# Kernel tuning notes

Hardware: AMD Instinct MI355X
Metric: run time of the kernel (lower is better)

The kernel has to match this reference:

```python
import jax, jax.numpy as jnp
import numpy as np
import math

B, T, N_EMBD, HEAD_SIZE = 8, 2048, 768, 128


def setup_inputs() -> dict:
    key = jax.random.key(0)
    ks = jax.random.split(key, 7)
    s = 0.02
    return {
        "x": jax.random.normal(ks[0], (B, T, N_EMBD), dtype=jnp.float32),
        "Wq": jax.random.normal(ks[1], (N_EMBD, HEAD_SIZE), dtype=jnp.float32) * s,
        "bq": jax.random.normal(ks[2], (HEAD_SIZE,), dtype=jnp.float32) * s,
        "Wk": jax.random.normal(ks[3], (N_EMBD, HEAD_SIZE), dtype=jnp.float32) * s,
        "bk": jax.random.normal(ks[4], (HEAD_SIZE,), dtype=jnp.float32) * s,
        "Wv": jax.random.normal(ks[5], (N_EMBD, HEAD_SIZE), dtype=jnp.float32) * s,
        "bv": jax.random.normal(ks[6], (HEAD_SIZE,), dtype=jnp.float32) * s,
    }


def reference(x, Wq, bq, Wk, bk, Wv, bv):
    # x: [B, T, n_embd]
    Tlen = x.shape[1]
    q = x @ Wq + bq  # [B, T, hs]
    k = x @ Wk + bk
    v = x @ Wv + bv
    scores = jnp.einsum('bqd,bkd->bqk', q, k)  # [B, T, T]
    causal = jnp.tril(jnp.ones((Tlen, Tlen), dtype=bool))
    # original masks with -inf first, then divides by sqrt(head_size); -inf/scale == -inf,
    # so mask-then-scale is mathematically identical.
    scores = jnp.where(causal, scores, -jnp.inf) / math.sqrt(q.shape[-1])
    weights = jax.nn.softmax(scores, axis=-1)
    # dropout p=0.0 (inference/reference) -> identity
    out = jnp.einsum('bqk,bkd->bqd', weights, v)  # [B, T, hs]
    return out
```

## Files before the change

kernel.cpp:

```cpp
#include <hip/hip_runtime.h>

#define B_ 8
#define T_ 2048
#define E_ 768
#define D_ 128
#define SCALE2 (0.08838834764831845f * 1.4426950408889634f)

typedef _Float16 h8 __attribute__((ext_vector_type(8)));
typedef _Float16 h4 __attribute__((ext_vector_type(4)));
typedef _Float16 h2 __attribute__((ext_vector_type(2)));
typedef float f4 __attribute__((ext_vector_type(4)));

typedef __attribute__((address_space(1))) unsigned int as1_u32;
typedef __attribute__((address_space(3))) unsigned int as3_u32;

__device__ __forceinline__ void gl_lds16(const void* g, void* l) {
    __builtin_amdgcn_global_load_lds((const as1_u32*)g, (as3_u32*)l, 16, 0, 0);
}

__global__ __launch_bounds__(256) void w_prep(
    const float* __restrict__ Wq, const float* __restrict__ Wk,
    const float* __restrict__ Wv, _Float16* __restrict__ Wh)
{
    __shared__ float tile[64][129];
    const int y = blockIdx.x / 12, kc = blockIdx.x % 12;
    const float* W = (y == 0) ? Wq : (y == 1) ? Wk : Wv;
    const int k0 = kc * 64, t = threadIdx.x;
#pragma unroll
    for (int i = 0; i < 32; ++i) {
        const int idx = i * 256 + t;
        tile[idx >> 7][idx & 127] = W[(size_t)(k0 + (idx >> 7)) * D_ + (idx & 127)];
    }
    __syncthreads();
    const int n = t >> 1, hf = t & 1;
#pragma unroll
    for (int j = 0; j < 4; ++j) {
        const int kk = hf * 32 + j * 8;
        h8 hv;
#pragma unroll
        for (int e = 0; e < 8; ++e) hv[e] = (_Float16)tile[kk + e][n];
        *(h8*)&Wh[(size_t)(y * 128 + n) * E_ + k0 + kk] = hv;
    }
}

__global__ __launch_bounds__(512, 1) void qkv_fused(
    const float* __restrict__ x, const _Float16* __restrict__ Wh,
    const float* __restrict__ bq, const float* __restrict__ bk,
    const float* __restrict__ bv,
    _Float16* __restrict__ Qh, _Float16* __restrict__ Kh,
    _Float16* __restrict__ Vt)
{
    __shared__ _Float16 As[2][64 * 64];
    __shared__ _Float16 Bs[2][384 * 64];

    const int t = threadIdx.x;
    const int lane = t & 63, w = t >> 6;
    const int quad = lane >> 4, col = lane & 15;
    const int m0 = blockIdx.x * 64;

    f4 acc[4][3];
#pragma unroll
    for (int mt = 0; mt < 4; ++mt)
#pragma unroll
        for (int nt = 0; nt < 3; ++nt) acc[mt][nt] = (f4){0.f, 0.f, 0.f, 0.f};

    const int brl = lane >> 3, bc = lane & 7;
    const int xr_ = t >> 3, xcb = (t & 7) * 8;

    float4 xv[2];

#define LOAD_X(kb)                                                          \
    {   const float* xr = &x[(size_t)(m0 + xr_) * E_ + (kb) + xcb];         \
        xv[0] = *(const float4*)(xr);                                       \
        xv[1] = *(const float4*)(xr + 4);                                   }

#define STAGE_B(dst, kb)                                                    \
    _Pragma("unroll")                                                       \
    for (int i = 0; i < 6; ++i) {                                           \
        const int R = w * 48 + i * 8;                                       \
        const int r = R + brl;                                              \
        gl_lds16(Wh + (size_t)r * E_ + (kb) + 8 * (bc ^ (r & 7)), &(dst)[R * 64]); }

#define WRITE_A(dst)                                                        \
    _Pragma("unroll")                                                       \
    for (int i = 0; i < 2; ++i) {                                           \
        h4 hv; hv[0] = (_Float16)xv[i].x; hv[1] = (_Float16)xv[i].y;        \
        hv[2] = (_Float16)xv[i].z; hv[3] = (_Float16)xv[i].w;               \
        const int kk4 = xcb + 4 * i;                                        \
        *(h4*)&(dst)[xr_ * 64 + (((kk4 >> 3) ^ (xr_ & 7)) << 3) + (kk4 & 7)] = hv; }

    LOAD_X(0);
    STAGE_B(Bs[0], 0);
    asm volatile("s_waitcnt vmcnt(6)" ::: "memory");
    WRITE_A(As[0]);
    asm volatile("s_waitcnt vmcnt(0) lgkmcnt(0)" ::: "memory");
    __builtin_amdgcn_s_barrier();

#pragma unroll 2
    for (int it = 0; it < 12; ++it) {
        const int c = it & 1;
        if (it < 11) {
            LOAD_X((it + 1) * 64);
            STAGE_B(Bs[c ^ 1], (it + 1) * 64);
        }
#pragma unroll
        for (int ks = 0; ks < 2; ++ks) {
            const int sc = ((ks << 2) + quad) ^ (col & 7);
            h8 a[4], bf[3];
#pragma unroll
            for (int mt = 0; mt < 4; ++mt)
                a[mt] = *(const h8*)&As[c][(mt * 16 + col) * 64 + (sc << 3)];
#pragma unroll
            for (int nt = 0; nt < 3; ++nt)
                bf[nt] = *(const h8*)&Bs[c][(w * 48 + nt * 16 + col) * 64 + (sc << 3)];
#pragma unroll
            for (int mt = 0; mt < 4; ++mt)
#pragma unroll
                for (int nt = 0; nt < 3; ++nt)
                    acc[mt][nt] = __builtin_amdgcn_mfma_f32_16x16x32_f16(
                        a[mt], bf[nt], acc[mt][nt], 0, 0, 0);
        }
        if (it < 11) {
            asm volatile("s_waitcnt vmcnt(6)" ::: "memory");
            WRITE_A(As[c ^ 1]);
            asm volatile("s_waitcnt vmcnt(0) lgkmcnt(0)" ::: "memory");
            __builtin_amdgcn_s_barrier();
        }
    }

    const float* bp[3] = {bq, bk, bv};
    _Float16* Cs = &Bs[0][0];
#pragma unroll
    for (int nt = 0; nt < 3; ++nt) {
        const int n16 = w * 48 + nt * 16;
        const int y = n16 >> 7, nl = n16 & 127;
        const float bb = bp[y][nl + col];
#pragma unroll
        for (int mt = 0; mt < 4; ++mt)
#pragma unroll
            for (int reg = 0; reg < 4; ++reg) {
                const int m = mt * 16 + quad * 4 + reg;
                Cs[m * 384 + n16 + col] = (_Float16)(acc[mt][nt][reg] + bb);
            }
    }
    __syncthreads();

    {
        const int m = t >> 3, seg = t & 7;
#pragma unroll
        for (int j = 0; j < 4; ++j) {
            const int n = seg * 8 + j * 64;
            const h8 v = *(const h8*)&Cs[m * 384 + n];
            if (n < 128) *(h8*)&Qh[(size_t)(m0 + m) * D_ + n] = v;
            else         *(h8*)&Kh[(size_t)(m0 + m) * D_ + (n - 128)] = v;
        }
    }
    {
        const int vn = t & 127, part = t >> 7;
        const int bidx = m0 >> 11, tt0 = m0 & 2047;
#pragma unroll
        for (int j = 0; j < 2; ++j) {
            const int ms = part * 16 + j * 8;
            h8 hv;
#pragma unroll
            for (int e = 0; e < 8; ++e) hv[e] = Cs[(ms + e) * 384 + 256 + vn];
            *(h8*)&Vt[((size_t)bidx * D_ + vn) * T_ + tt0 + ms] = hv;
        }
    }
#undef LOAD_X
#undef STAGE_B
#undef WRITE_A
}

__global__ __launch_bounds__(256, 2) void flash_attn(
    const _Float16* __restrict__ Qh,
    const _Float16* __restrict__ Kh,
    const _Float16* __restrict__ Vt,
    float* __restrict__ out)
{
    __shared__ __align__(16) char smem[70656];
    _Float16* Ks = (_Float16*)smem;
    _Float16* Vs = (_Float16*)(smem + 32768);
    _Float16* Pb = (_Float16*)(smem + 65536);

    const int t = threadIdx.x, lane = t & 63, w = t >> 6;
    const int quad = lane >> 4, col = lane & 15;
    const int id = blockIdx.x;
    const int b = id & 7;
    const int k6 = id >> 3;
    const int j32 = (k6 < 32) ? (63 - k6) : (k6 - 32);
    const int qw = w & 1, kh = w >> 1;
    const int qbase = j32 * 32;
    const int qrow0 = qbase + qw * 16;
    const int nk = (j32 >> 1) + 1;

    h8 qf[4];
    const _Float16* Qp = Qh + ((size_t)b * T_ + qrow0 + col) * D_ + quad * 8;
#pragma unroll
    for (int ks = 0; ks < 4; ++ks) qf[ks] = *(const h8*)(Qp + ks * 32);
    asm volatile("s_waitcnt vmcnt(0)" ::: "memory");

    f4 o[8];
#pragma unroll
    for (int i = 0; i < 8; ++i) o[i] = (f4){0.f, 0.f, 0.f, 0.f};
    float m_st = -1e30f, l_st = 0.f;

    const _Float16* Kb = Kh + (size_t)b * T_ * D_;
    const _Float16* Vb = Vt + (size_t)b * D_ * T_;
    const int krl = lane >> 4, kc = lane & 15;
    const int vrl = lane >> 3, vc = lane & 7;
    const int cx = col & 7;

    auto stage = [&](int buf, int kbase) __attribute__((always_inline)) {
        _Float16* KsB = Ks + buf * 8192;
        _Float16* VsB = Vs + buf * 8192;
#pragma unroll
        for (int i = 0; i < 4; ++i) {
            const int R = w * 16 + i * 4;
            const int r = R + krl;
            gl_lds16(Kb + (size_t)(kbase + r) * D_ + 8 * (kc ^ (r & 7)), KsB + R * D_);
        }
#pragma unroll
        for (int i = 0; i < 4; ++i) {
            const int R = w * 32 + i * 8;
            const int d = R + vrl;
            gl_lds16(Vb + (size_t)d * T_ + kbase + 8 * (vc ^ (d & 7)), VsB + R * 64);
        }
    };

    _Float16* Pw = Pb + w * 640;

    auto step = [&](int ti, int buf, bool mask) __attribute__((always_inline)) {
        const _Float16* KsB = Ks + buf * 8192;
        const _Float16* VsB = Vs + buf * 8192;

        f4 s[2];
        s[0] = (f4){0.f, 0.f, 0.f, 0.f};
        s[1] = (f4){0.f, 0.f, 0.f, 0.f};
        __builtin_amdgcn_s_setprio(1);
#pragma unroll
        for (int nt = 0; nt < 2; ++nt) {
            const int r = kh * 32 + nt * 16 + col;
#pragma unroll
            for (int ks = 0; ks < 4; ++ks) {
                const h8 kf = *(const h8*)(KsB + r * D_ + 8 * (((ks << 2) + quad) ^ cx));
                s[nt] = __builtin_amdgcn_mfma_f32_16x16x32_f16(kf, qf[ks], s[nt], 0, 0, 0);
            }
        }
        __builtin_amdgcn_s_setprio(0);

        const int qr = qrow0 + col;
        if (mask) {
#pragma unroll
            for (int nt = 0; nt < 2; ++nt) {
                const int key = ti * 64 + kh * 32 + nt * 16 + quad * 4;
#pragma unroll
                for (int reg = 0; reg < 4; ++reg) {
                    const float sv = s[nt][reg] * SCALE2;
                    s[nt][reg] = (key + reg <= qr) ? sv : -1e30f;
                }
            }
        } else {
#pragma unroll
            for (int nt = 0; nt < 2; ++nt)
#pragma unroll
                for (int reg = 0; reg < 4; ++reg) s[nt][reg] *= SCALE2;
        }

        float mloc = fmaxf(fmaxf(fmaxf(s[0][0], s[0][1]), fmaxf(s[0][2], s[0][3])),
                           fmaxf(fmaxf(s[1][0], s[1][1]), fmaxf(s[1][2], s[1][3])));
        mloc = fmaxf(mloc, __shfl_xor(mloc, 16));
        mloc = fmaxf(mloc, __shfl_xor(mloc, 32));

        if (__any((int)(mloc > m_st))) {
            const float mn = fmaxf(m_st, mloc);
            const float al = __builtin_amdgcn_exp2f(m_st - mn);
            m_st = mn;
            l_st *= al;
#pragma unroll
            for (int n2 = 0; n2 < 8; ++n2) o[n2] *= al;
        }

        float rs = 0.f;
#pragma unroll
        for (int nt = 0; nt < 2; ++nt)
#pragma unroll
            for (int reg = 0; reg < 4; ++reg) {
                const float p = __builtin_amdgcn_exp2f(s[nt][reg] - m_st);
                s[nt][reg] = p;
                rs += p;
            }
        rs += __shfl_xor(rs, 16);
        rs += __shfl_xor(rs, 32);
        l_st += rs;

#pragma unroll
        for (int nt = 0; nt < 2; ++nt) {
            h2 p0; p0[0] = (_Float16)s[nt][0]; p0[1] = (_Float16)s[nt][1];
            h2 p1; p1[0] = (_Float16)s[nt][2]; p1[1] = (_Float16)s[nt][3];
            *(h2*)&Pw[col * 40 + nt * 16 + quad * 4]     = p0;
            *(h2*)&Pw[col * 40 + nt * 16 + quad * 4 + 2] = p1;
        }
        const h8 pa = *(const h8*)&Pw[col * 40 + quad * 8];

        __builtin_amdgcn_s_setprio(1);
#pragma unroll
        for (int n2 = 0; n2 < 8; ++n2) {
            const int d = n2 * 16 + col;
            const h8 vf = *(const h8*)(VsB + d * 64 + 8 * ((kh * 4 + quad) ^ (d & 7)));
            o[n2] = __builtin_amdgcn_mfma_f32_16x16x32_f16(vf, pa, o[n2], 0, 0, 0);
        }
        __builtin_amdgcn_s_setprio(0);
    };

    stage(0, 0);
    const bool evenJ = ((j32 & 1) == 0);
    for (int ti = 0; ti < nk; ++ti) {
        const int cur = ti & 1;
        if (ti + 1 < nk) {
            stage(cur ^ 1, (ti + 1) << 6);
            asm volatile("s_waitcnt vmcnt(8)" ::: "memory");
        } else {
            asm volatile("s_waitcnt vmcnt(0)" ::: "memory");
        }
        __builtin_amdgcn_s_barrier();
        const bool last = (ti == nk - 1);
        if (!(last && evenJ && kh == 1)) {
            const bool mask = last && (kh == (j32 & 1));
            step(ti, cur, mask);
        }
        __builtin_amdgcn_s_barrier();
    }

    float* Os = (float*)smem;
    float* Mx = (float*)(smem + 16896);
    float* Lx = Mx + 32;
    const int qloc = qw * 16 + col;

    __syncthreads();
    if (kh == 1) {
        if (quad == 0) { Mx[qloc] = m_st; Lx[qloc] = l_st; }
#pragma unroll
        for (int n2 = 0; n2 < 8; ++n2)
#pragma unroll
            for (int reg = 0; reg < 4; ++reg)
                Os[qloc * 132 + n2 * 16 + quad * 4 + reg] = o[n2][reg];
    }
    __syncthreads();
    if (kh == 0) {
        const float m1 = Mx[qloc], l1 = Lx[qloc];
        const float mN = fmaxf(m_st, m1);
        const float a0 = __builtin_amdgcn_exp2f(m_st - mN);
        const float a1 = __builtin_amdgcn_exp2f(m1 - mN);
        const float inv = 1.0f / (l_st * a0 + l1 * a1);
#pragma unroll
        for (int n2 = 0; n2 < 8; ++n2)
#pragma unroll
            for (int reg = 0; reg < 4; ++reg) {
                const int d = n2 * 16 + quad * 4 + reg;
                Os[qloc * 132 + d] = (o[n2][reg] * a0 + Os[qloc * 132 + d] * a1) * inv;
            }
    }
    __syncthreads();
    {
        const int row = t >> 3, d0 = (t & 7) * 16;
        float* op = &out[((size_t)b * T_ + qbase + row) * D_ + d0];
#pragma unroll
        for (int j = 0; j < 4; ++j)
            *(float4*)(op + j * 4) = *(const float4*)&Os[row * 132 + d0 + j * 4];
    }
}

extern "C" void kernel_launch(void* const* d_in, const int* in_sizes, int n_in,
                              void* d_out, int out_size, void* d_ws, size_t ws_size,
                              hipStream_t stream) {
    const float* x  = (const float*)d_in[0];
    const float* Wq = (const float*)d_in[1];
    const float* bq = (const float*)d_in[2];
    const float* Wk = (const float*)d_in[3];
    const float* bk = (const float*)d_in[4];
    const float* Wv = (const float*)d_in[5];
    const float* bv = (const float*)d_in[6];

    _Float16* Qh = (_Float16*)d_ws;
    _Float16* Kh = Qh + (size_t)B_ * T_ * D_;
    _Float16* Vt = Kh + (size_t)B_ * T_ * D_;
    _Float16* Wh = (_Float16*)d_out;

    w_prep<<<dim3(36), dim3(256), 0, stream>>>(Wq, Wk, Wv, Wh);
    qkv_fused<<<dim3(B_ * T_ / 64), dim3(512), 0, stream>>>(
        x, Wh, bq, bk, bv, Qh, Kh, Vt);
    flash_attn<<<dim3(512), dim3(256), 0, stream>>>(Qh, Kh, Vt, (float*)d_out);
}
```

Baseline: 150.7 us.

## Load K/V fragments directly from global into registers, dropping LDS staging

```diff
diff --git a/kernel.cpp b/kernel.cpp
--- a/kernel.cpp
+++ b/kernel.cpp
@@ -178,10 +178,8 @@
     const _Float16* __restrict__ Vt,
     float* __restrict__ out)
 {
-    __shared__ __align__(16) char smem[70656];
-    _Float16* Ks = (_Float16*)smem;
-    _Float16* Vs = (_Float16*)(smem + 32768);
-    _Float16* Pb = (_Float16*)(smem + 65536);
+    __shared__ __align__(16) char smem[17408];
+    _Float16* Pb = (_Float16*)smem;
 
     const int t = threadIdx.x, lane = t & 63, w = t >> 6;
     const int quad = lane >> 4, col = lane & 15;
@@ -192,13 +190,12 @@
     const int qw = w & 1, kh = w >> 1;
     const int qbase = j32 * 32;
     const int qrow0 = qbase + qw * 16;
-    const int nk = (j32 >> 1) + 1;
+    const int gmax = (qrow0 + 15) >> 5;
 
     h8 qf[4];
     const _Float16* Qp = Qh + ((size_t)b * T_ + qrow0 + col) * D_ + quad * 8;
 #pragma unroll
     for (int ks = 0; ks < 4; ++ks) qf[ks] = *(const h8*)(Qp + ks * 32);
-    asm volatile("s_waitcnt vmcnt(0)" ::: "memory");
 
     f4 o[8];
 #pragma unroll
@@ -207,53 +204,44 @@
 
     const _Float16* Kb = Kh + (size_t)b * T_ * D_;
     const _Float16* Vb = Vt + (size_t)b * D_ * T_;
-    const int krl = lane >> 4, kc = lane & 15;
-    const int vrl = lane >> 3, vc = lane & 7;
-    const int cx = col & 7;
-
-    auto stage = [&](int buf, int kbase) __attribute__((always_inline)) {
-        _Float16* KsB = Ks + buf * 8192;
-        _Float16* VsB = Vs + buf * 8192;
-#pragma unroll
-        for (int i = 0; i < 4; ++i) {
-            const int R = w * 16 + i * 4;
-            const int r = R + krl;
-            gl_lds16(Kb + (size_t)(kbase + r) * D_ + 8 * (kc ^ (r & 7)), KsB + R * D_);
-        }
-#pragma unroll
-        for (int i = 0; i < 4; ++i) {
-            const int R = w * 32 + i * 8;
-            const int d = R + vrl;
-            gl_lds16(Vb + (size_t)d * T_ + kbase + 8 * (vc ^ (d & 7)), VsB + R * 64);
-        }
-    };
-
     _Float16* Pw = Pb + w * 640;
 
-    auto step = [&](int ti, int buf, bool mask) __attribute__((always_inline)) {
-        const _Float16* KsB = Ks + buf * 8192;
-        const _Float16* VsB = Vs + buf * 8192;
-
-        f4 s[2];
+    f4 s[2];
+    h8 pa;
+
+#define LOADK(dst, g_)                                                     \
+    _Pragma("unroll")                                                      \
+    for (int nt = 0; nt < 2; ++nt)                                         \
+    _Pragma("unroll")                                                      \
+    for (int ks = 0; ks < 4; ++ks)                                         \
+        dst[nt * 4 + ks] = *(const h8*)(Kb +                               \
+            (size_t)((g_) * 32 + nt * 16 + col) * D_ + (ks * 4 + quad) * 8);
+
+#define LOADV(dst, g_)                                                     \
+    _Pragma("unroll")                                                      \
+    for (int n2 = 0; n2 < 8; ++n2)                                         \
+        dst[n2] = *(const h8*)(Vb +                                        \
+            (size_t)(n2 * 16 + col) * T_ + (g_) * 32 + quad * 8);
+
+    auto qk = [&](const h8 (&kf)[8]) __attribute__((always_inline)) {
         s[0] = (f4){0.f, 0.f, 0.f, 0.f};
         s[1] = (f4){0.f, 0.f, 0.f, 0.f};
         __builtin_amdgcn_s_setprio(1);
 #pragma unroll
-        for (int nt = 0; nt < 2; ++nt) {
-            const int r = kh * 32 + nt * 16 + col;
-#pragma unroll
-            for (int ks = 0; ks < 4; ++ks) {
-                const h8 kf = *(const h8*)(KsB + r * D_ + 8 * (((ks << 2) + quad) ^ cx));
-                s[nt] = __builtin_amdgcn_mfma_f32_16x16x32_f16(kf, qf[ks], s[nt], 0, 0, 0);
-            }
-        }
+        for (int nt = 0; nt < 2; ++nt)
+#pragma unroll
+            for (int ks = 0; ks < 4; ++ks)
+                s[nt] = __builtin_amdgcn_mfma_f32_16x16x32_f16(
+                    kf[nt * 4 + ks], qf[ks], s[nt], 0, 0, 0);
         __builtin_amdgcn_s_setprio(0);
-
+    };
+
+    auto sm = [&](const int g) __attribute__((always_inline)) {
         const int qr = qrow0 + col;
-        if (mask) {
+        if (g == gmax) {
 #pragma unroll
             for (int nt = 0; nt < 2; ++nt) {
-                const int key = ti * 64 + kh * 32 + nt * 16 + quad * 4;
+                const int key = g * 32 + nt * 16 + quad * 4;
 #pragma unroll
                 for (int reg = 0; reg < 4; ++reg) {
                     const float sv = s[nt][reg] * SCALE2;
@@ -266,12 +254,10 @@
 #pragma unroll
                 for (int reg = 0; reg < 4; ++reg) s[nt][reg] *= SCALE2;
         }
-
         float mloc = fmaxf(fmaxf(fmaxf(s[0][0], s[0][1]), fmaxf(s[0][2], s[0][3])),
                            fmaxf(fmaxf(s[1][0], s[1][1]), fmaxf(s[1][2], s[1][3])));
         mloc = fmaxf(mloc, __shfl_xor(mloc, 16));
         mloc = fmaxf(mloc, __shfl_xor(mloc, 32));
-
         if (__any((int)(mloc > m_st))) {
             const float mn = fmaxf(m_st, mloc);
             const float al = __builtin_amdgcn_exp2f(m_st - mn);
@@ -280,7 +266,6 @@
 #pragma unroll
             for (int n2 = 0; n2 < 8; ++n2) o[n2] *= al;
         }
-
         float rs = 0.f;
 #pragma unroll
         for (int nt = 0; nt < 2; ++nt)
@@ -293,7 +278,6 @@
         rs += __shfl_xor(rs, 16);
         rs += __shfl_xor(rs, 32);
         l_st += rs;
-
 #pragma unroll
         for (int nt = 0; nt < 2; ++nt) {
             h2 p0; p0[0] = (_Float16)s[nt][0]; p0[1] = (_Float16)s[nt][1];
@@ -301,35 +285,35 @@
             *(h2*)&Pw[col * 40 + nt * 16 + quad * 4]     = p0;
             *(h2*)&Pw[col * 40 + nt * 16 + quad * 4 + 2] = p1;
         }
-        const h8 pa = *(const h8*)&Pw[col * 40 + quad * 8];
-
+        pa = *(const h8*)&Pw[col * 40 + quad * 8];
+    };
+
+    auto pv = [&](const h8 (&vf)[8]) __attribute__((always_inline)) {
         __builtin_amdgcn_s_setprio(1);
 #pragma unroll
-        for (int n2 = 0; n2 < 8; ++n2) {
-            const int d = n2 * 16 + col;
-            const h8 vf = *(const h8*)(VsB + d * 64 + 8 * ((kh * 4 + quad) ^ (d & 7)));
-            o[n2] = __builtin_amdgcn_mfma_f32_16x16x32_f16(vf, pa, o[n2], 0, 0, 0);
-        }
+        for (int n2 = 0; n2 < 8; ++n2)
+            o[n2] = __builtin_amdgcn_mfma_f32_16x16x32_f16(vf[n2], pa, o[n2], 0, 0, 0);
         __builtin_amdgcn_s_setprio(0);
     };
 
-    stage(0, 0);
-    const bool evenJ = ((j32 & 1) == 0);
-    for (int ti = 0; ti < nk; ++ti) {
-        const int cur = ti & 1;
-        if (ti + 1 < nk) {
-            stage(cur ^ 1, (ti + 1) << 6);
-            asm volatile("s_waitcnt vmcnt(8)" ::: "memory");
-        } else {
-            asm volatile("s_waitcnt vmcnt(0)" ::: "memory");
-        }
-        __builtin_amdgcn_s_barrier();
-        const bool last = (ti == nk - 1);
-        if (!(last && evenJ && kh == 1)) {
-            const bool mask = last && (kh == (j32 & 1));
-            step(ti, cur, mask);
-        }
-        __builtin_amdgcn_s_barrier();
+    h8 ka[8], kb2[8], va[8], vb2[8];
+    int g = kh;
+    if (g <= gmax) {
+        LOADK(ka, g);
+        LOADV(va, g);
+#define BODY(KC, VC, KN, VN)                                               \
+        qk(KC);                                                            \
+        if (g + 2 <= gmax) { LOADK(KN, g + 2); }                           \
+        sm(g);                                                             \
+        pv(VC);                                                            \
+        if (g + 2 <= gmax) { LOADV(VN, g + 2); }                           \
+        g += 2;                                                            \
+        if (g > gmax) break;
+        while (true) {
+            BODY(ka, va, kb2, vb2)
+            BODY(kb2, vb2, ka, va)
+        }
+#undef BODY
     }
 
     float* Os = (float*)smem;
@@ -369,6 +353,8 @@
         for (int j = 0; j < 4; ++j)
             *(float4*)(op + j * 4) = *(const float4*)&Os[row * 132 + d0 + j * 4];
     }
+#undef LOADK
+#undef LOADV
 }
 
 extern "C" void kernel_launch(void* const* d_in, const int* in_sizes, int n_in,
```

Measured after the change: 175.8 us. 16.6% more time.
